# Optimization experiments

Hardware: AMD Instinct MI355X
Metric: run time of the kernel (lower is better)

## Reference

```python
import jax, jax.numpy as jnp
import numpy as np

ALPHA = 0.5  # leakage
RHO = 0.99
SCALE = 0.9


def setup_inputs() -> dict:
    key = jax.random.key(0)
    k1, k2, k3 = jax.random.split(key, 3)
    T, B, I, H = 512, 64, 256, 2048
    x = jax.random.normal(k1, (T, B, I), dtype=jnp.float32)
    initial_state = jnp.zeros((B, H), dtype=jnp.float32)
    # kernel: uniform in [-scale, scale]
    W_in = jax.random.uniform(k2, (H, I), dtype=jnp.float32, minval=-SCALE, maxval=SCALE)
    # recurrent: normal, rescaled so spectral radius ~= rho (circular-law estimate)
    W_hat = jax.random.normal(k3, (H, H), dtype=jnp.float32) * (RHO / jnp.sqrt(jnp.float32(H)))
    return {"x": x, "initial_state": initial_state, "W_in": W_in, "W_hat": W_hat}


def reference(x, initial_state, W_in, W_hat):
    # Precompute input projections for all timesteps: [T, B, H]
    u = jnp.einsum('tbi,hi->tbh', x, W_in)

    def step(state, u_t):
        h_t = jnp.tanh(u_t + state @ W_hat.T)
        state = (1.0 - ALPHA) * state + ALPHA * h_t
        return state, state

    _, states = jax.lax.scan(step, initial_state, u)
    return states  # [T, B, H]
```

## Files before the change

kernel.cpp:

```cpp
#include <hip/hip_runtime.h>

typedef __attribute__((ext_vector_type(8))) short short8;
typedef __attribute__((ext_vector_type(4))) float floatx4;

#define TT 512
#define BB 64
#define II 256
#define HH 2048

#define MFMA(a, b, c) __builtin_amdgcn_mfma_f32_16x16x32_bf16(a, b, c, 0, 0, 0)

__device__ __forceinline__ short f2bf(float f) {
  unsigned u = __builtin_bit_cast(unsigned, f);
  u = (u + 0x7fffu + ((u >> 16) & 1u)) >> 16;
  return (short)u;
}
__device__ __forceinline__ float bf2f(short s) {
  unsigned u = ((unsigned)(unsigned short)s) << 16;
  return __builtin_bit_cast(float, u);
}

__global__ __launch_bounds__(64) void pack_what(const float* __restrict__ What,
                                                short8* __restrict__ PWhi,
                                                short8* __restrict__ PWlo) {
  const int ntile = blockIdx.x >> 6;
  const int kb = blockIdx.x & 63;
  const int L = threadIdx.x;
  const int lm = L & 15, lq = L >> 4;
  const float* p = What + (size_t)(ntile * 16 + lm) * HH + kb * 32 + lq * 8;
  short8 hi, lo;
#pragma unroll
  for (int j = 0; j < 8; ++j) {
    float f = p[j];
    short h = f2bf(f);
    hi[j] = h;
    lo[j] = f2bf(f - bf2f(h));
  }
  const size_t o = (size_t)blockIdx.x * 64 + L;
  PWhi[o] = hi;
  PWlo[o] = lo;
}

__global__ __launch_bounds__(256) void prep_state(const float* __restrict__ s0,
                                                  short* __restrict__ Shi,
                                                  short* __restrict__ Slo) {
  int i = blockIdx.x * 256 + threadIdx.x;
  float f = s0[i];
  short h = f2bf(f);
  Shi[i] = h;
  Slo[i] = f2bf(f - bf2f(h));
}

__global__ __launch_bounds__(256) void ugemm(const float* __restrict__ X,
                                             const float* __restrict__ Win,
                                             float* __restrict__ U) {
  const int w = threadIdx.x >> 6;
  const int L = threadIdx.x & 63;
  const int lm = L & 15, lq = L >> 4;
  const int m0 = blockIdx.x * 128 + (w >> 1) * 64;
  const int n0 = blockIdx.y * 64 + (w & 1) * 32;

  short8 Bhi[2][8], Blo[2][8];
#pragma unroll
  for (int nt = 0; nt < 2; ++nt)
#pragma unroll
    for (int kt = 0; kt < 8; ++kt) {
      const float* p = Win + (n0 + nt * 16 + lm) * II + kt * 32 + lq * 8;
      short8 hi, lo;
#pragma unroll
      for (int j = 0; j < 8; ++j) {
        float f = p[j];
        short h = f2bf(f);
        hi[j] = h;
        lo[j] = f2bf(f - bf2f(h));
      }
      Bhi[nt][kt] = hi;
      Blo[nt][kt] = lo;
    }

#pragma unroll 1
  for (int mt = 0; mt < 4; ++mt) {
    short8 Ahi[8], Alo[8];
    const int r = m0 + mt * 16 + lm;
#pragma unroll
    for (int kt = 0; kt < 8; ++kt) {
      const float* p = X + (size_t)r * II + kt * 32 + lq * 8;
      short8 hi, lo;
#pragma unroll
      for (int j = 0; j < 8; ++j) {
        float f = p[j];
        short h = f2bf(f);
        hi[j] = h;
        lo[j] = f2bf(f - bf2f(h));
      }
      Ahi[kt] = hi;
      Alo[kt] = lo;
    }
#pragma unroll
    for (int nt = 0; nt < 2; ++nt) {
      floatx4 acc = {0.f, 0.f, 0.f, 0.f};
#pragma unroll
      for (int kt = 0; kt < 8; ++kt) {
        acc = MFMA(Ahi[kt], Bhi[nt][kt], acc);
        acc = MFMA(Ahi[kt], Blo[nt][kt], acc);
        acc = MFMA(Alo[kt], Bhi[nt][kt], acc);
      }
#pragma unroll
      for (int rr = 0; rr < 4; ++rr) {
        int row = m0 + mt * 16 + lq * 4 + rr;
        int col = n0 + nt * 16 + lm;
        U[(size_t)row * HH + col] = acc[rr];
      }
    }
  }
}

__global__ __launch_bounds__(256) void step_kernel(
    const short8* __restrict__ PWhi, const short8* __restrict__ PWlo,
    const short* __restrict__ Sh, const short* __restrict__ Sl,
    short* __restrict__ Nh, short* __restrict__ Nl,
    float* __restrict__ out_t) {
  __shared__ float red[4][32][17];
  const int w = threadIdx.x >> 6;
  const int L = threadIdx.x & 63;
  const int lm = L & 15, lq = L >> 4;
  const int mhalf = blockIdx.x & 1;
  const int ntile = blockIdx.x >> 1;
  const int mbase = mhalf * 32;
  const int kw = w * 512;

  floatx4 acc0 = {0.f, 0.f, 0.f, 0.f};
  floatx4 acc1 = {0.f, 0.f, 0.f, 0.f};
  const size_t wbase = ((size_t)ntile * 64 + (kw >> 5)) * 64 + L;
#pragma unroll
  for (int kt = 0; kt < 16; ++kt) {
    short8 bh = PWhi[wbase + (size_t)kt * 64];
    short8 bl = PWlo[wbase + (size_t)kt * 64];
    const int k0 = kw + kt * 32 + lq * 8;
    short8 a0h = *(const short8*)(Sh + (mbase + lm) * HH + k0);
    short8 a0l = *(const short8*)(Sl + (mbase + lm) * HH + k0);
    short8 a1h = *(const short8*)(Sh + (mbase + 16 + lm) * HH + k0);
    short8 a1l = *(const short8*)(Sl + (mbase + 16 + lm) * HH + k0);
    acc0 = MFMA(a0h, bh, acc0);
    acc0 = MFMA(a0h, bl, acc0);
    acc0 = MFMA(a0l, bh, acc0);
    acc1 = MFMA(a1h, bh, acc1);
    acc1 = MFMA(a1h, bl, acc1);
    acc1 = MFMA(a1l, bh, acc1);
  }

#pragma unroll
  for (int r = 0; r < 4; ++r) {
    red[w][lq * 4 + r][lm] = acc0[r];
    red[w][16 + lq * 4 + r][lm] = acc1[r];
  }
  __syncthreads();

#pragma unroll
  for (int p = 0; p < 2; ++p) {
    const int e = threadIdx.x + p * 256;
    const int row = e >> 4, col = e & 15;
    const int gb = mbase + row;
    const int gh = ntile * 16 + col;
    const int idx = gb * HH + gh;
    float z = out_t[idx];
#pragma unroll
    for (int ww = 0; ww < 4; ++ww) z += red[ww][row][col];
    const float sp = bf2f(Sh[idx]) + bf2f(Sl[idx]);
    const float hv = tanhf(z);
    const float sn = 0.5f * (sp + hv);
    out_t[idx] = sn;
    const short shi = f2bf(sn);
    Nh[idx] = shi;
    Nl[idx] = f2bf(sn - bf2f(shi));
  }
}

extern "C" void kernel_launch(void* const* d_in, const int* in_sizes, int n_in,
                              void* d_out, int out_size, void* d_ws, size_t ws_size,
                              hipStream_t stream) {
  const float* x = (const float*)d_in[0];
  const float* s0 = (const float*)d_in[1];
  const float* Win = (const float*)d_in[2];
  const float* What = (const float*)d_in[3];
  float* out = (float*)d_out;

  short8* PWhi = (short8*)d_ws;
  short8* PWlo = PWhi + (size_t)HH * HH / 8;
  short* SAh = (short*)(PWlo + (size_t)HH * HH / 8);
  short* SAl = SAh + BB * HH;
  short* SBh = SAl + BB * HH;
  short* SBl = SBh + BB * HH;

  pack_what<<<8192, 64, 0, stream>>>(What, PWhi, PWlo);
  prep_state<<<512, 256, 0, stream>>>(s0, SAh, SAl);
  ugemm<<<dim3(256, 32), 256, 0, stream>>>(x, Win, out);

  for (int t = 0; t < TT; ++t) {
    const short* curH = (t & 1) ? SBh : SAh;
    const short* curL = (t & 1) ? SBl : SAl;
    short* nxtH = (t & 1) ? SAh : SBh;
    short* nxtL = (t & 1) ? SAl : SBl;
    step_kernel<<<256, 256, 0, stream>>>(PWhi, PWlo, curH, curL, nxtH, nxtL,
                                         out + (size_t)t * BB * HH);
  }
}
```

Baseline: 7.843 ms.

## Fuse timestep loop into persistent cooperative kernel with flag-based grid barrier

New measurement: 18.47 ms. 136% more time.

```diff
diff --git a/kernel.cpp b/kernel.cpp
--- a/kernel.cpp
+++ b/kernel.cpp
@@ -7,6 +7,7 @@
 #define BB 64
 #define II 256
 #define HH 2048
+#define BH (BB * HH)
 
 #define MFMA(a, b, c) __builtin_amdgcn_mfma_f32_16x16x32_bf16(a, b, c, 0, 0, 0)
 
@@ -43,8 +44,10 @@
 
 __global__ __launch_bounds__(256) void prep_state(const float* __restrict__ s0,
                                                   short* __restrict__ Shi,
-                                                  short* __restrict__ Slo) {
+                                                  short* __restrict__ Slo,
+                                                  unsigned* __restrict__ flags) {
   int i = blockIdx.x * 256 + threadIdx.x;
+  if (i < 4096) flags[i] = 0;
   float f = s0[i];
   short h = f2bf(f);
   Shi[i] = h;
@@ -115,64 +118,103 @@
   }
 }
 
-__global__ __launch_bounds__(256) void step_kernel(
+__global__ __launch_bounds__(256, 1) void recurrence(
     const short8* __restrict__ PWhi, const short8* __restrict__ PWlo,
-    const short* __restrict__ Sh, const short* __restrict__ Sl,
-    short* __restrict__ Nh, short* __restrict__ Nl,
-    float* __restrict__ out_t) {
+    short* __restrict__ SH, short* __restrict__ SL,
+    float* __restrict__ out, unsigned* __restrict__ flags) {
   __shared__ float red[4][32][17];
-  const int w = threadIdx.x >> 6;
-  const int L = threadIdx.x & 63;
+  const int tid = threadIdx.x;
+  const int w = tid >> 6;
+  const int L = tid & 63;
   const int lm = L & 15, lq = L >> 4;
   const int mhalf = blockIdx.x & 1;
   const int ntile = blockIdx.x >> 1;
   const int mbase = mhalf * 32;
   const int kw = w * 512;
 
-  floatx4 acc0 = {0.f, 0.f, 0.f, 0.f};
-  floatx4 acc1 = {0.f, 0.f, 0.f, 0.f};
-  const size_t wbase = ((size_t)ntile * 64 + (kw >> 5)) * 64 + L;
+  short8 Wh[16], Wl[16];
+  const size_t wb = ((size_t)ntile * 64 + (kw >> 5)) * 64 + L;
 #pragma unroll
   for (int kt = 0; kt < 16; ++kt) {
-    short8 bh = PWhi[wbase + (size_t)kt * 64];
-    short8 bl = PWlo[wbase + (size_t)kt * 64];
-    const int k0 = kw + kt * 32 + lq * 8;
-    short8 a0h = *(const short8*)(Sh + (mbase + lm) * HH + k0);
-    short8 a0l = *(const short8*)(Sl + (mbase + lm) * HH + k0);
-    short8 a1h = *(const short8*)(Sh + (mbase + 16 + lm) * HH + k0);
-    short8 a1l = *(const short8*)(Sl + (mbase + 16 + lm) * HH + k0);
-    acc0 = MFMA(a0h, bh, acc0);
-    acc0 = MFMA(a0h, bl, acc0);
-    acc0 = MFMA(a0l, bh, acc0);
-    acc1 = MFMA(a1h, bh, acc1);
-    acc1 = MFMA(a1h, bl, acc1);
-    acc1 = MFMA(a1l, bh, acc1);
-  }
-
-#pragma unroll
-  for (int r = 0; r < 4; ++r) {
-    red[w][lq * 4 + r][lm] = acc0[r];
-    red[w][16 + lq * 4 + r][lm] = acc1[r];
-  }
-  __syncthreads();
-
-#pragma unroll
-  for (int p = 0; p < 2; ++p) {
-    const int e = threadIdx.x + p * 256;
-    const int row = e >> 4, col = e & 15;
-    const int gb = mbase + row;
-    const int gh = ntile * 16 + col;
-    const int idx = gb * HH + gh;
-    float z = out_t[idx];
-#pragma unroll
-    for (int ww = 0; ww < 4; ++ww) z += red[ww][row][col];
-    const float sp = bf2f(Sh[idx]) + bf2f(Sl[idx]);
-    const float hv = tanhf(z);
-    const float sn = 0.5f * (sp + hv);
-    out_t[idx] = sn;
-    const short shi = f2bf(sn);
-    Nh[idx] = shi;
-    Nl[idx] = f2bf(sn - bf2f(shi));
+    Wh[kt] = PWhi[wb + (size_t)kt * 64];
+    Wl[kt] = PWlo[wb + (size_t)kt * 64];
+  }
+
+  const int r0 = (mbase + lm) * HH;
+  const int r1 = (mbase + 16 + lm) * HH;
+  const int ecol = tid & 15;
+  const int e0row = tid >> 4;
+  const int e1row = 16 + e0row;
+  const int idx0 = (mbase + e0row) * HH + ntile * 16 + ecol;
+  const int idx1 = (mbase + e1row) * HH + ntile * 16 + ecol;
+
+  int slot = 0;
+  for (int t = 0; t < TT; ++t) {
+    int nslot = slot + 1;
+    if (nslot == 3) nslot = 0;
+    const short* curH = SH + slot * BH;
+    const short* curL = SL + slot * BH;
+    short* nxtH = SH + nslot * BH;
+    short* nxtL = SL + nslot * BH;
+    float* ot = out + (size_t)t * BH;
+
+    float u0 = ot[idx0], u1 = ot[idx1];
+    float sp0 = bf2f(curH[idx0]) + bf2f(curL[idx0]);
+    float sp1 = bf2f(curH[idx1]) + bf2f(curL[idx1]);
+
+    floatx4 a00 = {0.f, 0.f, 0.f, 0.f}, a01 = a00, a02 = a00;
+    floatx4 a10 = a00, a11 = a00, a12 = a00;
+#pragma unroll
+    for (int kt = 0; kt < 16; ++kt) {
+      const int k0 = kw + kt * 32 + lq * 8;
+      short8 x0h = *(const short8*)(curH + r0 + k0);
+      short8 x0l = *(const short8*)(curL + r0 + k0);
+      short8 x1h = *(const short8*)(curH + r1 + k0);
+      short8 x1l = *(const short8*)(curL + r1 + k0);
+      a00 = MFMA(x0h, Wh[kt], a00);
+      a10 = MFMA(x1h, Wh[kt], a10);
+      a01 = MFMA(x0h, Wl[kt], a01);
+      a11 = MFMA(x1h, Wl[kt], a11);
+      a02 = MFMA(x0l, Wh[kt], a02);
+      a12 = MFMA(x1l, Wh[kt], a12);
+    }
+    floatx4 s0v = a00 + a01 + a02;
+    floatx4 s1v = a10 + a11 + a12;
+
+#pragma unroll
+    for (int r = 0; r < 4; ++r) {
+      red[w][lq * 4 + r][lm] = s0v[r];
+      red[w][16 + lq * 4 + r][lm] = s1v[r];
+    }
+    __syncthreads();
+
+    float z0 = u0, z1 = u1;
+#pragma unroll
+    for (int ww = 0; ww < 4; ++ww) {
+      z0 += red[ww][e0row][ecol];
+      z1 += red[ww][e1row][ecol];
+    }
+    const float sn0 = 0.5f * (sp0 + tanhf(z0));
+    const float sn1 = 0.5f * (sp1 + tanhf(z1));
+    ot[idx0] = sn0;
+    ot[idx1] = sn1;
+    const short h0 = f2bf(sn0), h1 = f2bf(sn1);
+    nxtH[idx0] = h0;
+    nxtL[idx0] = f2bf(sn0 - bf2f(h0));
+    nxtH[idx1] = h1;
+    nxtL[idx1] = f2bf(sn1 - bf2f(h1));
+
+    __syncthreads();
+    const unsigned g = (unsigned)(t + 1);
+    if (tid == 0)
+      __hip_atomic_store(&flags[(unsigned)blockIdx.x * 16u], g,
+                         __ATOMIC_RELEASE, __HIP_MEMORY_SCOPE_AGENT);
+    while (__hip_atomic_load(&flags[(unsigned)tid * 16u],
+                             __ATOMIC_ACQUIRE, __HIP_MEMORY_SCOPE_AGENT) < g)
+      __builtin_amdgcn_s_sleep(1);
+    __syncthreads();
+
+    slot = nslot;
   }
 }
 
@@ -187,21 +229,18 @@
 
   short8* PWhi = (short8*)d_ws;
   short8* PWlo = PWhi + (size_t)HH * HH / 8;
-  short* SAh = (short*)(PWlo + (size_t)HH * HH / 8);
-  short* SAl = SAh + BB * HH;
-  short* SBh = SAl + BB * HH;
-  short* SBl = SBh + BB * HH;
+  short* SH = (short*)(PWlo + (size_t)HH * HH / 8);
+  short* SL = SH + 3 * BH;
+  unsigned* flags = (unsigned*)(SL + 3 * BH);
 
   pack_what<<<8192, 64, 0, stream>>>(What, PWhi, PWlo);
-  prep_state<<<512, 256, 0, stream>>>(s0, SAh, SAl);
+  prep_state<<<512, 256, 0, stream>>>(s0, SH, SL, flags);
   ugemm<<<dim3(256, 32), 256, 0, stream>>>(x, Win, out);
 
-  for (int t = 0; t < TT; ++t) {
-    const short* curH = (t & 1) ? SBh : SAh;
-    const short* curL = (t & 1) ? SBl : SAl;
-    short* nxtH = (t & 1) ? SAh : SBh;
-    short* nxtL = (t & 1) ? SAl : SBl;
-    step_kernel<<<256, 256, 0, stream>>>(PWhi, PWlo, curH, curL, nxtH, nxtL,
-                                         out + (size_t)t * BB * HH);
-  }
-}
+  void* kargs[] = {&PWhi, &PWlo, &SH, &SL, &out, &flags};
+  hipError_t ce = hipLaunchCooperativeKernel(
+      reinterpret_cast<void*>(&recurrence), dim3(256), dim3(256), kargs, 0, stream);
+  if (ce != hipSuccess) {
+    recurrence<<<256, 256, 0, stream>>>(PWhi, PWlo, SH, SL, out, flags);
+  }
+}
```

## Split step kernel K-reduction across 16 waves and break MFMA dependency chains

Applied to the files above, without the earlier changes.

After: 6.280 ms. 1.25x faster.

```diff
diff --git a/kernel.cpp b/kernel.cpp
--- a/kernel.cpp
+++ b/kernel.cpp
@@ -7,6 +7,7 @@
 #define BB 64
 #define II 256
 #define HH 2048
+#define BH (BB * HH)
 
 #define MFMA(a, b, c) __builtin_amdgcn_mfma_f32_16x16x32_bf16(a, b, c, 0, 0, 0)
 
@@ -115,64 +116,71 @@
   }
 }
 
-__global__ __launch_bounds__(256) void step_kernel(
+__global__ __launch_bounds__(1024, 4) void step_kernel(
     const short8* __restrict__ PWhi, const short8* __restrict__ PWlo,
     const short* __restrict__ Sh, const short* __restrict__ Sl,
     short* __restrict__ Nh, short* __restrict__ Nl,
     float* __restrict__ out_t) {
-  __shared__ float red[4][32][17];
-  const int w = threadIdx.x >> 6;
-  const int L = threadIdx.x & 63;
+  __shared__ float red[16][32][17];
+  const int tid = threadIdx.x;
+  const int w = tid >> 6;
+  const int L = tid & 63;
   const int lm = L & 15, lq = L >> 4;
   const int mhalf = blockIdx.x & 1;
   const int ntile = blockIdx.x >> 1;
   const int mbase = mhalf * 32;
-  const int kw = w * 512;
-
-  floatx4 acc0 = {0.f, 0.f, 0.f, 0.f};
-  floatx4 acc1 = {0.f, 0.f, 0.f, 0.f};
+  const int kw = w * 128;
+
+  const int ecol = tid & 15;
+  const int erow = tid >> 4;
+  float u0 = 0.f, sp0 = 0.f;
+  int idx0 = 0;
+  if (tid < 512) {
+    idx0 = (mbase + erow) * HH + ntile * 16 + ecol;
+    u0 = out_t[idx0];
+    sp0 = bf2f(Sh[idx0]) + bf2f(Sl[idx0]);
+  }
+
+  floatx4 a00 = {0.f, 0.f, 0.f, 0.f}, a01 = a00, a02 = a00;
+  floatx4 a10 = a00, a11 = a00, a12 = a00;
   const size_t wbase = ((size_t)ntile * 64 + (kw >> 5)) * 64 + L;
-#pragma unroll
-  for (int kt = 0; kt < 16; ++kt) {
+  const int r0 = (mbase + lm) * HH;
+  const int r1 = (mbase + 16 + lm) * HH;
+#pragma unroll
+  for (int kt = 0; kt < 4; ++kt) {
     short8 bh = PWhi[wbase + (size_t)kt * 64];
     short8 bl = PWlo[wbase + (size_t)kt * 64];
     const int k0 = kw + kt * 32 + lq * 8;
-    short8 a0h = *(const short8*)(Sh + (mbase + lm) * HH + k0);
-    short8 a0l = *(const short8*)(Sl + (mbase + lm) * HH + k0);
-    short8 a1h = *(const short8*)(Sh + (mbase + 16 + lm) * HH + k0);
-    short8 a1l = *(const short8*)(Sl + (mbase + 16 + lm) * HH + k0);
-    acc0 = MFMA(a0h, bh, acc0);
-    acc0 = MFMA(a0h, bl, acc0);
-    acc0 = MFMA(a0l, bh, acc0);
-    acc1 = MFMA(a1h, bh, acc1);
-    acc1 = MFMA(a1h, bl, acc1);
-    acc1 = MFMA(a1l, bh, acc1);
-  }
+    short8 a0h = *(const short8*)(Sh + r0 + k0);
+    short8 a0l = *(const short8*)(Sl + r0 + k0);
+    short8 a1h = *(const short8*)(Sh + r1 + k0);
+    short8 a1l = *(const short8*)(Sl + r1 + k0);
+    a00 = MFMA(a0h, bh, a00);
+    a10 = MFMA(a1h, bh, a10);
+    a01 = MFMA(a0h, bl, a01);
+    a11 = MFMA(a1h, bl, a11);
+    a02 = MFMA(a0l, bh, a02);
+    a12 = MFMA(a1l, bh, a12);
+  }
+  floatx4 s0v = a00 + a01 + a02;
+  floatx4 s1v = a10 + a11 + a12;
 
 #pragma unroll
   for (int r = 0; r < 4; ++r) {
-    red[w][lq * 4 + r][lm] = acc0[r];
-    red[w][16 + lq * 4 + r][lm] = acc1[r];
+    red[w][lq * 4 + r][lm] = s0v[r];
+    red[w][16 + lq * 4 + r][lm] = s1v[r];
   }
   __syncthreads();
 
-#pragma unroll
-  for (int p = 0; p < 2; ++p) {
-    const int e = threadIdx.x + p * 256;
-    const int row = e >> 4, col = e & 15;
-    const int gb = mbase + row;
-    const int gh = ntile * 16 + col;
-    const int idx = gb * HH + gh;
-    float z = out_t[idx];
-#pragma unroll
-    for (int ww = 0; ww < 4; ++ww) z += red[ww][row][col];
-    const float sp = bf2f(Sh[idx]) + bf2f(Sl[idx]);
-    const float hv = tanhf(z);
-    const float sn = 0.5f * (sp + hv);
-    out_t[idx] = sn;
+  if (tid < 512) {
+    float z = u0;
+#pragma unroll
+    for (int ww = 0; ww < 16; ++ww) z += red[ww][erow][ecol];
+    const float sn = 0.5f * (sp0 + tanhf(z));
+    out_t[idx0] = sn;
     const short shi = f2bf(sn);
-    Nh[idx] = shi;
-    Nl[idx] = f2bf(sn - bf2f(shi));
+    Nh[idx0] = shi;
+    Nl[idx0] = f2bf(sn - bf2f(shi));
   }
 }
 
@@ -188,9 +196,9 @@
   short8* PWhi = (short8*)d_ws;
   short8* PWlo = PWhi + (size_t)HH * HH / 8;
   short* SAh = (short*)(PWlo + (size_t)HH * HH / 8);
-  short* SAl = SAh + BB * HH;
-  short* SBh = SAl + BB * HH;
-  short* SBl = SBh + BB * HH;
+  short* SAl = SAh + BH;
+  short* SBh = SAl + BH;
+  short* SBl = SBh + BH;
 
   pack_what<<<8192, 64, 0, stream>>>(What, PWhi, PWlo);
   prep_state<<<512, 256, 0, stream>>>(s0, SAh, SAl);
@@ -201,7 +209,7 @@
     const short* curL = (t & 1) ? SBl : SAl;
     short* nxtH = (t & 1) ? SAh : SBh;
     short* nxtL = (t & 1) ? SAl : SBl;
-    step_kernel<<<256, 256, 0, stream>>>(PWhi, PWlo, curH, curL, nxtH, nxtL,
-                                         out + (size_t)t * BB * HH);
-  }
-}
+    step_kernel<<<256, 1024, 0, stream>>>(PWhi, PWlo, curH, curL, nxtH, nxtL,
+                                          out + (size_t)t * BH);
+  }
+}
```
